# Kernel tuning notes

Hardware: AMD Instinct MI355X
Metric: run time of the kernel (lower is better)

The kernel has to match this reference:

```python
import jax, jax.numpy as jnp
import numpy as np

B, T, C, H, W = 1, 8, 128, 64, 64
F = 64  # num_feat


def setup_inputs() -> dict:
    key = jax.random.key(0)
    ks = jax.random.split(key, 8)
    return {
        "input1": jax.random.normal(ks[0], (B, T, C, H, W), jnp.float32),
        "input2": jax.random.normal(ks[1], (B, T, C, H, W), jnp.float32),
        "W1": jax.random.normal(ks[2], (F, C), jnp.float32) * 0.05,
        "b1": jax.random.normal(ks[3], (F,), jnp.float32) * 0.05,
        "W2": jax.random.normal(ks[4], (F, C), jnp.float32) * 0.05,
        "b2": jax.random.normal(ks[5], (F,), jnp.float32) * 0.05,
        "W3": jax.random.normal(ks[6], (F, C), jnp.float32) * 0.05,
        "b3": jax.random.normal(ks[7], (F,), jnp.float32) * 0.05,
    }


def reference(input1, input2, W1, b1, W2, b2, W3, b3):
    # act == 0 (ReLU branch). Conv1d(kernel=1) == per-position linear projection.
    b, t, c, h, w = input1.shape
    n = h * w
    x1 = input1.reshape(b, t, c, n)  # matches transpose(1,2).reshape then frame slice
    x2 = input2.reshape(b, t, c, n)
    q = jnp.einsum('fc,btcn->btnf', W1, x1) + b1          # [B,T,N,F]
    k = jnp.einsum('fc,btcn->btnf', W2, x2) + b2          # [B,T,N,F]
    g = jnp.einsum('fc,btcn->btnf', W3, x1) + b3          # [B,T,N,F]
    scores = jax.nn.relu(jnp.einsum('btnf,btmf->btnm', q, k))  # [B,T,N,N]
    out = jnp.einsum('btnm,btmf->btnf', scores, g)        # [B,T,N,F]
    # view([B,H,W,F]).permute(0,3,1,2), stacked over T -> [B,T,F,H,W]
    return out.reshape(b, t, h, w, -1).transpose(0, 1, 4, 2, 3)
```

## Files before the change

kernel.cpp:

```cpp
#include <hip/hip_runtime.h>
#include <hip/hip_bf16.h>

constexpr int T = 8;
constexpr int C = 128;
constexpr int N = 4096;
constexpr int F = 64;

typedef __bf16 bf16x8 __attribute__((ext_vector_type(8)));
typedef float  f32x4  __attribute__((ext_vector_type(4)));

__global__ __launch_bounds__(256) void prep_w_kernel(
    const float* __restrict__ W1, const float* __restrict__ W2,
    const float* __restrict__ W3, __bf16* __restrict__ Wb)
{
    int i = blockIdx.x * 256 + threadIdx.x;
    const float* Ws[3] = {W1, W2, W3};
    int p = i >> 13, r = i & 8191;
    Wb[i] = (__bf16)Ws[p][r];
}

__global__ __launch_bounds__(256) void zero_out_kernel(float* __restrict__ out)
{
    int i = blockIdx.x * 256 + threadIdx.x;
    ((f32x4*)out)[i] = (f32x4){0.f, 0.f, 0.f, 0.f};
}

__global__ __launch_bounds__(256) void proj_kernel(
    const float* __restrict__ x1, const float* __restrict__ x2,
    const __bf16* __restrict__ Wb,
    const float* __restrict__ b1, const float* __restrict__ b2,
    const float* __restrict__ b3,
    __bf16* __restrict__ Qb, __bf16* __restrict__ Kb, __bf16* __restrict__ Gw)
{
    const int t  = blockIdx.x >> 6;
    const int nb = blockIdx.x & 63;
    const int n0 = nb * 64;

    constexpr int XS = C + 8;
    __shared__ __bf16 Xt1[64 * XS];
    __shared__ __bf16 Xt2[64 * XS];

    const int tid = threadIdx.x;
#pragma unroll
    for (int rep = 0; rep < 32; ++rep) {
        int idx = rep * 256 + tid;
        int c = idx >> 6, nl = idx & 63;
        size_t goff = ((size_t)t * C + c) * (size_t)N + n0 + nl;
        Xt1[nl * XS + c] = (__bf16)x1[goff];
        Xt2[nl * XS + c] = (__bf16)x2[goff];
    }
    __syncthreads();

    const int wave = tid >> 6, lane = tid & 63;
    const int quad = lane >> 4, l16 = lane & 15;

    bf16x8 a1[4], a2[4];
#pragma unroll
    for (int cc = 0; cc < 4; ++cc) {
        a1[cc] = *(const bf16x8*)&Xt1[(wave * 16 + l16) * XS + cc * 32 + quad * 8];
        a2[cc] = *(const bf16x8*)&Xt2[(wave * 16 + l16) * XS + cc * 32 + quad * 8];
    }

#pragma unroll
    for (int p = 0; p < 2; ++p) {
        const __bf16* W    = Wb + (size_t)p * F * C;
        const float*  bias = p ? b2 : b1;
        __bf16*       O    = p ? Kb : Qb;

        f32x4 acc[4];
#pragma unroll
        for (int ft = 0; ft < 4; ++ft) acc[ft] = (f32x4){0.f, 0.f, 0.f, 0.f};
#pragma unroll
        for (int cc = 0; cc < 4; ++cc) {
#pragma unroll
            for (int ft = 0; ft < 4; ++ft) {
                bf16x8 b = *(const bf16x8*)&W[(ft * 16 + l16) * C + cc * 32 + quad * 8];
                bf16x8 a = p ? a2[cc] : a1[cc];
                acc[ft] = __builtin_amdgcn_mfma_f32_16x16x32_bf16(a, b, acc[ft], 0, 0, 0);
            }
        }
#pragma unroll
        for (int ft = 0; ft < 4; ++ft) {
            int f = ft * 16 + l16;
            float bv = bias[f];
#pragma unroll
            for (int r = 0; r < 4; ++r) {
                int n = n0 + wave * 16 + quad * 4 + r;
                O[((size_t)t * N + n) * F + f] = (__bf16)(acc[ft][r] + bv);
            }
        }
    }

    {
        const __bf16* W3b = Wb + (size_t)2 * F * C;
        bf16x8 wa[4];
#pragma unroll
        for (int cc = 0; cc < 4; ++cc)
            wa[cc] = *(const bf16x8*)&W3b[(wave * 16 + l16) * C + cc * 32 + quad * 8];

        f32x4 acc[4];
#pragma unroll
        for (int nt = 0; nt < 4; ++nt) acc[nt] = (f32x4){0.f, 0.f, 0.f, 0.f};
#pragma unroll
        for (int cc = 0; cc < 4; ++cc) {
#pragma unroll
            for (int nt = 0; nt < 4; ++nt) {
                bf16x8 b = *(const bf16x8*)&Xt1[(nt * 16 + l16) * XS + cc * 32 + quad * 8];
                acc[nt] = __builtin_amdgcn_mfma_f32_16x16x32_bf16(wa[cc], b, acc[nt], 0, 0, 0);
            }
        }
#pragma unroll
        for (int nt = 0; nt < 4; ++nt) {
#pragma unroll
            for (int r = 0; r < 4; ++r) {
                int f = wave * 16 + quad * 4 + r;
                int n = n0 + nt * 16 + l16;
                Gw[((size_t)t * F + f) * (size_t)N + n] = (__bf16)(acc[nt][r] + b3[f]);
            }
        }
    }
}

constexpr int KSPLIT = 2;

__global__ __launch_bounds__(256) void attn_kernel(
    const __bf16* __restrict__ Qb, const __bf16* __restrict__ Kb,
    const __bf16* __restrict__ Gw, float* __restrict__ out)
{
    const int ks = blockIdx.x & (KSPLIT - 1);
    const int qb = (blockIdx.x >> 1) & 63;
    const int t  = blockIdx.x >> 7;
    const int q0 = qb * 64;

    constexpr int KS = 72;
    __shared__ __bf16 Kt[64 * KS];
    __shared__ __bf16 Gt[64 * KS];
    __shared__ __bf16 Sb[64 * KS];

    const int tid = threadIdx.x, wave = tid >> 6, lane = tid & 63;
    const int quad = lane >> 4, l16 = lane & 15;

    bf16x8 qf[2];
    {
        const __bf16* qrow = &Qb[((size_t)t * N + q0 + wave * 16 + l16) * F];
        qf[0] = *(const bf16x8*)&qrow[quad * 8];
        qf[1] = *(const bf16x8*)&qrow[32 + quad * 8];
    }

    f32x4 oacc[4];
#pragma unroll
    for (int ft = 0; ft < 4; ++ft) oacc[ft] = (f32x4){0.f, 0.f, 0.f, 0.f};

    const int kb_lo = ks * (N / 64 / KSPLIT);
    const int kb_hi = kb_lo + (N / 64 / KSPLIT);

    for (int kb = kb_lo; kb < kb_hi; ++kb) {
        const int k0 = kb * 64;
        __syncthreads();
#pragma unroll
        for (int rep = 0; rep < 2; ++rep) {
            int u  = rep * 256 + tid;
            int r8 = u >> 3, c8 = (u & 7) * 8;
            *(bf16x8*)&Kt[r8 * KS + c8] =
                *(const bf16x8*)&Kb[((size_t)t * N + k0 + r8) * F + c8];
            *(bf16x8*)&Gt[r8 * KS + c8] =
                *(const bf16x8*)&Gw[((size_t)t * F + r8) * (size_t)N + k0 + c8];
        }
        __syncthreads();

#pragma unroll
        for (int nt = 0; nt < 4; ++nt) {
            f32x4 s = (f32x4){0.f, 0.f, 0.f, 0.f};
            bf16x8 b0 = *(const bf16x8*)&Kt[(nt * 16 + l16) * KS + quad * 8];
            bf16x8 b1 = *(const bf16x8*)&Kt[(nt * 16 + l16) * KS + 32 + quad * 8];
            s = __builtin_amdgcn_mfma_f32_16x16x32_bf16(qf[0], b0, s, 0, 0, 0);
            s = __builtin_amdgcn_mfma_f32_16x16x32_bf16(qf[1], b1, s, 0, 0, 0);
#pragma unroll
            for (int r = 0; r < 4; ++r) {
                float v = fmaxf(s[r], 0.f);
                Sb[(wave * 16 + quad * 4 + r) * KS + nt * 16 + l16] = (__bf16)v;
            }
        }
        bf16x8 s0 = *(const bf16x8*)&Sb[(wave * 16 + l16) * KS + quad * 8];
        bf16x8 s1 = *(const bf16x8*)&Sb[(wave * 16 + l16) * KS + 32 + quad * 8];
#pragma unroll
        for (int ft = 0; ft < 4; ++ft) {
            bf16x8 g0 = *(const bf16x8*)&Gt[(ft * 16 + l16) * KS + quad * 8];
            bf16x8 g1 = *(const bf16x8*)&Gt[(ft * 16 + l16) * KS + 32 + quad * 8];
            oacc[ft] = __builtin_amdgcn_mfma_f32_16x16x32_bf16(g0, s0, oacc[ft], 0, 0, 0);
            oacc[ft] = __builtin_amdgcn_mfma_f32_16x16x32_bf16(g1, s1, oacc[ft], 0, 0, 0);
        }
    }

#pragma unroll
    for (int ft = 0; ft < 4; ++ft) {
#pragma unroll
        for (int r = 0; r < 4; ++r) {
            int f = ft * 16 + quad * 4 + r;
            int q = q0 + wave * 16 + l16;
            unsafeAtomicAdd(&out[((size_t)t * F + f) * (size_t)N + q], oacc[ft][r]);
        }
    }
}

extern "C" void kernel_launch(void* const* d_in, const int* in_sizes, int n_in,
                              void* d_out, int out_size, void* d_ws, size_t ws_size,
                              hipStream_t stream) {
    const float* x1 = (const float*)d_in[0];
    const float* x2 = (const float*)d_in[1];
    const float* W1 = (const float*)d_in[2];
    const float* b1 = (const float*)d_in[3];
    const float* W2 = (const float*)d_in[4];
    const float* b2 = (const float*)d_in[5];
    const float* W3 = (const float*)d_in[6];
    const float* b3 = (const float*)d_in[7];
    float* out = (float*)d_out;

    __bf16* Qb = (__bf16*)d_ws;
    __bf16* Kb = Qb + (size_t)T * N * F;
    __bf16* Gw = Kb + (size_t)T * N * F;
    __bf16* Wb = Gw + (size_t)T * N * F;

    prep_w_kernel<<<dim3(3 * F * C / 256), dim3(256), 0, stream>>>(W1, W2, W3, Wb);
    proj_kernel<<<dim3(T * (N / 64)), dim3(256), 0, stream>>>(
        x1, x2, Wb, b1, b2, b3, Qb, Kb, Gw);
    zero_out_kernel<<<dim3(T * F * N / 4 / 256), dim3(256), 0, stream>>>(out);
    attn_kernel<<<dim3(T * (N / 64) * KSPLIT), dim3(256), 0, stream>>>(Qb, Kb, Gw, out);
}
```

Measured before the change: 179.5 us.

## Double query tile per block, prefetch K/G tiles into registers, transpose S compute

The attention kernel now handles 128 queries per block (32 per wave) instead of 64, so each K and G tile staged in shared memory is reused across twice as many queries and the number of blocks is halved. The next K/G tile is loaded into registers while the current one is being computed, overlapping global loads with MFMA work. The score MFMA operands are swapped so each lane can write its ReLU'd scores as one packed 4-wide store. The costs are more registers per thread, a larger score buffer in shared memory, and only 512 blocks, which may leave the GPU less fully occupied.

```diff
diff --git a/kernel.cpp b/kernel.cpp
--- a/kernel.cpp
+++ b/kernel.cpp
@@ -7,6 +7,7 @@
 constexpr int F = 64;
 
 typedef __bf16 bf16x8 __attribute__((ext_vector_type(8)));
+typedef __bf16 bf16x4 __attribute__((ext_vector_type(4)));
 typedef float  f32x4  __attribute__((ext_vector_type(4)));
 
 __global__ __launch_bounds__(256) void prep_w_kernel(
@@ -128,79 +129,108 @@
     const __bf16* __restrict__ Gw, float* __restrict__ out)
 {
     const int ks = blockIdx.x & (KSPLIT - 1);
-    const int qb = (blockIdx.x >> 1) & 63;
-    const int t  = blockIdx.x >> 7;
-    const int q0 = qb * 64;
+    const int qb = (blockIdx.x / KSPLIT) & 31;
+    const int t  = blockIdx.x / (KSPLIT * 32);
+    const int q0 = qb * 128;
 
     constexpr int KS = 72;
     __shared__ __bf16 Kt[64 * KS];
     __shared__ __bf16 Gt[64 * KS];
-    __shared__ __bf16 Sb[64 * KS];
+    __shared__ __bf16 Sb[128 * KS];
 
     const int tid = threadIdx.x, wave = tid >> 6, lane = tid & 63;
     const int quad = lane >> 4, l16 = lane & 15;
 
-    bf16x8 qf[2];
-    {
-        const __bf16* qrow = &Qb[((size_t)t * N + q0 + wave * 16 + l16) * F];
-        qf[0] = *(const bf16x8*)&qrow[quad * 8];
-        qf[1] = *(const bf16x8*)&qrow[32 + quad * 8];
-    }
-
-    f32x4 oacc[4];
-#pragma unroll
-    for (int ft = 0; ft < 4; ++ft) oacc[ft] = (f32x4){0.f, 0.f, 0.f, 0.f};
+    bf16x8 qf[2][2];
+#pragma unroll
+    for (int qg = 0; qg < 2; ++qg) {
+        const __bf16* qrow = &Qb[((size_t)t * N + q0 + wave * 32 + qg * 16 + l16) * F];
+        qf[qg][0] = *(const bf16x8*)&qrow[quad * 8];
+        qf[qg][1] = *(const bf16x8*)&qrow[32 + quad * 8];
+    }
+
+    f32x4 oacc[4][2];
+#pragma unroll
+    for (int ft = 0; ft < 4; ++ft)
+#pragma unroll
+        for (int qg = 0; qg < 2; ++qg) oacc[ft][qg] = (f32x4){0.f, 0.f, 0.f, 0.f};
 
     const int kb_lo = ks * (N / 64 / KSPLIT);
     const int kb_hi = kb_lo + (N / 64 / KSPLIT);
 
+    const int r8a = tid >> 3,          c8a = (tid & 7) * 8;
+    const int r8b = (tid + 256) >> 3,  c8b = c8a;
+
+    bf16x8 kv0, kv1, gv0, gv1;
+    {
+        const int k0 = kb_lo * 64;
+        kv0 = *(const bf16x8*)&Kb[((size_t)t * N + k0 + r8a) * F + c8a];
+        kv1 = *(const bf16x8*)&Kb[((size_t)t * N + k0 + r8b) * F + c8b];
+        gv0 = *(const bf16x8*)&Gw[((size_t)t * F + r8a) * (size_t)N + k0 + c8a];
+        gv1 = *(const bf16x8*)&Gw[((size_t)t * F + r8b) * (size_t)N + k0 + c8b];
+    }
+
     for (int kb = kb_lo; kb < kb_hi; ++kb) {
-        const int k0 = kb * 64;
         __syncthreads();
-#pragma unroll
-        for (int rep = 0; rep < 2; ++rep) {
-            int u  = rep * 256 + tid;
-            int r8 = u >> 3, c8 = (u & 7) * 8;
-            *(bf16x8*)&Kt[r8 * KS + c8] =
-                *(const bf16x8*)&Kb[((size_t)t * N + k0 + r8) * F + c8];
-            *(bf16x8*)&Gt[r8 * KS + c8] =
-                *(const bf16x8*)&Gw[((size_t)t * F + r8) * (size_t)N + k0 + c8];
-        }
+        *(bf16x8*)&Kt[r8a * KS + c8a] = kv0;
+        *(bf16x8*)&Kt[r8b * KS + c8b] = kv1;
+        *(bf16x8*)&Gt[r8a * KS + c8a] = gv0;
+        *(bf16x8*)&Gt[r8b * KS + c8b] = gv1;
         __syncthreads();
 
+        if (kb + 1 < kb_hi) {
+            const int k0 = (kb + 1) * 64;
+            kv0 = *(const bf16x8*)&Kb[((size_t)t * N + k0 + r8a) * F + c8a];
+            kv1 = *(const bf16x8*)&Kb[((size_t)t * N + k0 + r8b) * F + c8b];
+            gv0 = *(const bf16x8*)&Gw[((size_t)t * F + r8a) * (size_t)N + k0 + c8a];
+            gv1 = *(const bf16x8*)&Gw[((size_t)t * F + r8b) * (size_t)N + k0 + c8b];
+        }
+
 #pragma unroll
         for (int nt = 0; nt < 4; ++nt) {
-            f32x4 s = (f32x4){0.f, 0.f, 0.f, 0.f};
-            bf16x8 b0 = *(const bf16x8*)&Kt[(nt * 16 + l16) * KS + quad * 8];
-            bf16x8 b1 = *(const bf16x8*)&Kt[(nt * 16 + l16) * KS + 32 + quad * 8];
-            s = __builtin_amdgcn_mfma_f32_16x16x32_bf16(qf[0], b0, s, 0, 0, 0);
-            s = __builtin_amdgcn_mfma_f32_16x16x32_bf16(qf[1], b1, s, 0, 0, 0);
-#pragma unroll
-            for (int r = 0; r < 4; ++r) {
-                float v = fmaxf(s[r], 0.f);
-                Sb[(wave * 16 + quad * 4 + r) * KS + nt * 16 + l16] = (__bf16)v;
-            }
-        }
-        bf16x8 s0 = *(const bf16x8*)&Sb[(wave * 16 + l16) * KS + quad * 8];
-        bf16x8 s1 = *(const bf16x8*)&Sb[(wave * 16 + l16) * KS + 32 + quad * 8];
+            bf16x8 k0f = *(const bf16x8*)&Kt[(nt * 16 + l16) * KS + quad * 8];
+            bf16x8 k1f = *(const bf16x8*)&Kt[(nt * 16 + l16) * KS + 32 + quad * 8];
+#pragma unroll
+            for (int qg = 0; qg < 2; ++qg) {
+                f32x4 s = (f32x4){0.f, 0.f, 0.f, 0.f};
+                s = __builtin_amdgcn_mfma_f32_16x16x32_bf16(k0f, qf[qg][0], s, 0, 0, 0);
+                s = __builtin_amdgcn_mfma_f32_16x16x32_bf16(k1f, qf[qg][1], s, 0, 0, 0);
+                bf16x4 sp;
+#pragma unroll
+                for (int r = 0; r < 4; ++r) sp[r] = (__bf16)fmaxf(s[r], 0.f);
+                *(bf16x4*)&Sb[(wave * 32 + qg * 16 + l16) * KS + nt * 16 + quad * 4] = sp;
+            }
+        }
+
+        bf16x8 sf[2][2];
+#pragma unroll
+        for (int qg = 0; qg < 2; ++qg) {
+            const __bf16* srow = &Sb[(wave * 32 + qg * 16 + l16) * KS];
+            sf[qg][0] = *(const bf16x8*)&srow[quad * 8];
+            sf[qg][1] = *(const bf16x8*)&srow[32 + quad * 8];
+        }
 #pragma unroll
         for (int ft = 0; ft < 4; ++ft) {
             bf16x8 g0 = *(const bf16x8*)&Gt[(ft * 16 + l16) * KS + quad * 8];
             bf16x8 g1 = *(const bf16x8*)&Gt[(ft * 16 + l16) * KS + 32 + quad * 8];
-            oacc[ft] = __builtin_amdgcn_mfma_f32_16x16x32_bf16(g0, s0, oacc[ft], 0, 0, 0);
-            oacc[ft] = __builtin_amdgcn_mfma_f32_16x16x32_bf16(g1, s1, oacc[ft], 0, 0, 0);
-        }
-    }
-
-#pragma unroll
-    for (int ft = 0; ft < 4; ++ft) {
-#pragma unroll
-        for (int r = 0; r < 4; ++r) {
-            int f = ft * 16 + quad * 4 + r;
-            int q = q0 + wave * 16 + l16;
-            unsafeAtomicAdd(&out[((size_t)t * F + f) * (size_t)N + q], oacc[ft][r]);
-        }
-    }
+#pragma unroll
+            for (int qg = 0; qg < 2; ++qg) {
+                oacc[ft][qg] = __builtin_amdgcn_mfma_f32_16x16x32_bf16(g0, sf[qg][0], oacc[ft][qg], 0, 0, 0);
+                oacc[ft][qg] = __builtin_amdgcn_mfma_f32_16x16x32_bf16(g1, sf[qg][1], oacc[ft][qg], 0, 0, 0);
+            }
+        }
+    }
+
+#pragma unroll
+    for (int ft = 0; ft < 4; ++ft)
+#pragma unroll
+        for (int qg = 0; qg < 2; ++qg)
+#pragma unroll
+            for (int r = 0; r < 4; ++r) {
+                int f = ft * 16 + quad * 4 + r;
+                int q = q0 + wave * 32 + qg * 16 + l16;
+                unsafeAtomicAdd(&out[((size_t)t * F + f) * (size_t)N + q], oacc[ft][qg][r]);
+            }
 }
 
 extern "C" void kernel_launch(void* const* d_in, const int* in_sizes, int n_in,
@@ -225,5 +255,5 @@
     proj_kernel<<<dim3(T * (N / 64)), dim3(256), 0, stream>>>(
         x1, x2, Wb, b1, b2, b3, Qb, Kb, Gw);
     zero_out_kernel<<<dim3(T * F * N / 4 / 256), dim3(256), 0, stream>>>(out);
-    attn_kernel<<<dim3(T * (N / 64) * KSPLIT), dim3(256), 0, stream>>>(Qb, Kb, Gw, out);
-}
+    attn_kernel<<<dim3(T * 32 * KSPLIT), dim3(256), 0, stream>>>(Qb, Kb, Gw, out);
+}
```

Measured after the change: 162.3 us. -9.6%, faster.
